# Optimization experiments

Measured on AMD Instinct MI355X. Metric: run time of the kernel, lower is better.

## Reference

```python
import jax, jax.numpy as jnp
import numpy as np

B, C, C2, E = 4, 1024, 1024, 1024
D = 1024          # context_size (d_q = d_kv)
NH = 16           # module's n_heads arg -> actual head_dim after the quirky view
G = D // NH       # effective number of head groups = 64


def setup_inputs() -> dict:
    key = jax.random.key(0)
    ks = jax.random.split(key, 6)
    s = 0.02
    return {
        "x1": jax.random.normal(ks[0], (B, C, E), dtype=jnp.float32),
        "x2": jax.random.normal(ks[1], (B, C2, E), dtype=jnp.float32),
        "W_q": jax.random.normal(ks[2], (E, D), dtype=jnp.float32) * s,
        "W_k": jax.random.normal(ks[3], (E, D), dtype=jnp.float32) * s,
        "W_v": jax.random.normal(ks[4], (E, D), dtype=jnp.float32) * s,
        "W_o": jax.random.normal(ks[5], (D, D), dtype=jnp.float32) * s,
    }


def _split_heads(t):
    # (B, S, D) -> view (B, S, G, NH) -> transpose(1,2) -> (B, G, S, NH)
    b, s, _ = t.shape
    return jnp.transpose(t.reshape(b, s, G, NH), (0, 2, 1, 3))


def reference(x1, x2, W_q, W_k, W_v, W_o):
    Q = _split_heads(x1 @ W_q)   # (B, G, C, NH)
    K = _split_heads(x2 @ W_k)   # (B, G, C2, NH)
    V = _split_heads(x2 @ W_v)   # (B, G, C2, NH)
    scale = 1.0 / jnp.sqrt(jnp.asarray(NH, dtype=Q.dtype))
    scores = jnp.einsum("bgqh,bgkh->bgqk", Q, K) * scale  # (B, G, C, C2)
    w = jax.nn.softmax(scores, axis=-1)
    out = jnp.einsum("bgqk,bgkh->bgqh", w, V)             # (B, G, C, NH)
    out = jnp.transpose(out, (0, 2, 1, 3)).reshape(B, C, D)
    return out @ W_o  # dropout p=0 -> identity
```

## Files before the change

### kernel.cpp

```cpp
#include <hip/hip_runtime.h>


typedef _Float16 f16x8 __attribute__((ext_vector_type(8)));
typedef _Float16 f16x4 __attribute__((ext_vector_type(4)));
typedef _Float16 f16x2 __attribute__((ext_vector_type(2)));
typedef float    f32x4 __attribute__((ext_vector_type(4)));
typedef float    f32x16 __attribute__((ext_vector_type(16)));

#define GLOAD_LDS16(gp, lp)                                              \
    __builtin_amdgcn_global_load_lds(                                    \
        (const __attribute__((address_space(1))) void*)(gp),             \
        (__attribute__((address_space(3))) void*)(lp), 16, 0, 0)

static __device__ __forceinline__ f16x8 pack8f(const float* p) {
    f16x2 a = __builtin_bit_cast(f16x2, __builtin_amdgcn_cvt_pkrtz(p[0], p[1]));
    f16x2 b = __builtin_bit_cast(f16x2, __builtin_amdgcn_cvt_pkrtz(p[2], p[3]));
    f16x2 c = __builtin_bit_cast(f16x2, __builtin_amdgcn_cvt_pkrtz(p[4], p[5]));
    f16x2 d = __builtin_bit_cast(f16x2, __builtin_amdgcn_cvt_pkrtz(p[6], p[7]));
    f16x8 r;
    r[0] = a[0]; r[1] = a[1]; r[2] = b[0]; r[3] = b[1];
    r[4] = c[0]; r[5] = c[1]; r[6] = d[0]; r[7] = d[1];
    return r;
}

__global__ __launch_bounds__(256) void prep_kernel(
        const float* __restrict__ x1, const float* __restrict__ x2,
        const float* __restrict__ W0, const float* __restrict__ W1,
        const float* __restrict__ W2, const float* __restrict__ W3,
        _Float16* __restrict__ y1, _Float16* __restrict__ y2,
        _Float16* __restrict__ T0, _Float16* __restrict__ T1,
        _Float16* __restrict__ T2, _Float16* __restrict__ T3) {
    int bx = blockIdx.x, tid = threadIdx.x;
    if (bx < 8192) {
        int i = bx * 256 + tid;
        const float* x = (i < 1048576) ? x1 : x2;
        _Float16* y = (i < 1048576) ? y1 : y2;
        int j = i & 1048575;
        float4 v = ((const float4*)x)[j];
        f16x4 h = { (_Float16)v.x, (_Float16)v.y, (_Float16)v.z, (_Float16)v.w };
        ((f16x4*)y)[j] = h;
    } else {
        int z = (bx - 8192) >> 10;
        const float* W = (z == 0) ? W0 : (z == 1) ? W1 : (z == 2) ? W2 : W3;
        _Float16* WT = (z == 0) ? T0 : (z == 1) ? T1 : (z == 2) ? T2 : T3;
        int t = (bx - 8192) & 1023;
        int c0 = (t & 31) * 32, r0 = (t >> 5) * 32;
        __shared__ float tile[32][33];
        int tx = tid & 31, ty = tid >> 5;
#pragma unroll
        for (int i = 0; i < 32; i += 8)
            tile[ty + i][tx] = W[(r0 + ty + i) * 1024 + (c0 + tx)];
        __syncthreads();
#pragma unroll
        for (int i = 0; i < 32; i += 8)
            WT[(c0 + ty + i) * 1024 + (r0 + tx)] = (_Float16)tile[tx][ty + i];
    }
}

template <int MT, bool OUTF32>
static __device__ __forceinline__ void gemm_body(const _Float16* __restrict__ Atile,
                                                 const _Float16* __restrict__ BTtile,
                                                 void* __restrict__ Ctile,
                                                 _Float16* As, _Float16* Bs) {
    constexpr int AF = MT / 32;
    const int tid = threadIdx.x, lane = tid & 63, wave = tid >> 6;
    const int wm = wave >> 1, wn = wave & 1;
    const int col = lane & 15, quad = lane >> 4;

    f32x4 acc[AF][4];
#pragma unroll
    for (int i = 0; i < AF; i++)
#pragma unroll
        for (int j = 0; j < 4; j++) acc[i][j] = (f32x4){0.f, 0.f, 0.f, 0.f};

    const int srow = wave * 8 + (lane >> 3);
    const int sch = (lane & 7) * 8;
    const _Float16* Ag = Atile + (size_t)srow * 1024 + sch;
    const _Float16* Bg = BTtile + (size_t)srow * 1024 + sch;
    _Float16* Asl = As + wave * 512;
    _Float16* Bsl = Bs + wave * 512;

    for (int kt = 0; kt < 16; kt++) {
        __syncthreads();
#pragma unroll
        for (int c = 0; c < AF; c++)
            GLOAD_LDS16(Ag + (size_t)(c * 32) * 1024 + kt * 64, Asl + c * 2048);
#pragma unroll
        for (int c = 0; c < 4; c++)
            GLOAD_LDS16(Bg + (size_t)(c * 32) * 1024 + kt * 64, Bsl + c * 2048);
        __syncthreads();
#pragma unroll
        for (int ki = 0; ki < 2; ki++) {
            f16x8 af[AF], bf[4];
#pragma unroll
            for (int i = 0; i < AF; i++)
                af[i] = *(const f16x8*)(As + (wm * (MT / 2) + i * 16 + col) * 64 + ki * 32 + quad * 8);
#pragma unroll
            for (int j = 0; j < 4; j++)
                bf[j] = *(const f16x8*)(Bs + (wn * 64 + j * 16 + col) * 64 + ki * 32 + quad * 8);
#pragma unroll
            for (int i = 0; i < AF; i++)
#pragma unroll
                for (int j = 0; j < 4; j++)
                    acc[i][j] = __builtin_amdgcn_mfma_f32_16x16x32_f16(af[i], bf[j], acc[i][j], 0, 0, 0);
        }
    }

#pragma unroll
    for (int i = 0; i < AF; i++)
#pragma unroll
        for (int ii = 0; ii < 4; ii++) {
            int row = wm * (MT / 2) + i * 16 + quad * 4 + ii;
#pragma unroll
            for (int j = 0; j < 4; j++) {
                int cc = wn * 64 + j * 16 + col;
                if (OUTF32) ((float*)Ctile)[(size_t)row * 1024 + cc] = acc[i][j][ii];
                else ((_Float16*)Ctile)[(size_t)row * 1024 + cc] = (_Float16)acc[i][j][ii];
            }
        }
}

__global__ __launch_bounds__(256, 3) void gemm_qkv_kernel(
        const _Float16* __restrict__ x1h, const _Float16* __restrict__ x2h,
        const _Float16* __restrict__ WqT, const _Float16* __restrict__ WkvT,
        _Float16* __restrict__ Qh, _Float16* __restrict__ Kh, _Float16* __restrict__ Vh) {
    __shared__ _Float16 As[128 * 64], Bs[128 * 64];
    int gx = blockIdx.x;
    const _Float16 *A, *BT;
    _Float16* C;
    int m0, n0;
    if (gx < 256) {
        m0 = (gx >> 3) * 128; n0 = (gx & 7) * 128;
        A = x1h; BT = WqT + (size_t)n0 * 1024; C = Qh + n0;
    } else {
        int idx = gx - 256;
        m0 = (idx >> 4) * 128;
        int nb = idx & 15;
        n0 = nb * 128;
        A = x2h; BT = WkvT + (size_t)n0 * 1024;
        C = (nb < 8) ? (Kh + n0) : (Vh + (n0 - 1024));
    }
    gemm_body<128, false>(A + (size_t)m0 * 1024, BT, (void*)(C + (size_t)m0 * 1024), As, Bs);
}

__global__ __launch_bounds__(256, 4) void gemm_wo_kernel(const _Float16* __restrict__ Ah,
                                                         const _Float16* __restrict__ WoT,
                                                         float* __restrict__ out) {
    __shared__ _Float16 As[64 * 64], Bs[128 * 64];
    int gx = blockIdx.x;
    int m0 = (gx >> 3) * 64, n0 = (gx & 7) * 128;
    gemm_body<64, true>(Ah + (size_t)m0 * 1024, WoT + (size_t)n0 * 1024,
                        (void*)(out + (size_t)m0 * 1024 + n0), As, Bs);
}

__global__ __launch_bounds__(256, 8) void attn_kernel(const _Float16* __restrict__ Qh,
                                                      const _Float16* __restrict__ Kh,
                                                      const _Float16* __restrict__ Vh,
                                                      _Float16* __restrict__ Ah) {
    int pair = blockIdx.y;
    int b = pair >> 6, g = pair & 63;
    __shared__ _Float16 KA[2048];
    __shared__ _Float16 VA[2048];
    __shared__ _Float16 ones[8];

    const _Float16* Kg = Kh + (size_t)(b * 1024) * 1024 + g * 16;
    const _Float16* Vg = Vh + (size_t)(b * 1024) * 1024 + g * 16;
    int tid = threadIdx.x;
    if (tid < 8) ones[tid] = (_Float16)1.f;

    int lane = tid & 63, wave = tid >> 6;
    int n = lane & 31, h5 = lane >> 5;
    int q0 = blockIdx.x * 128 + wave * 32;

    f16x8 qf;
    {
        f16x8 t = *(const f16x8*)(Qh + (size_t)(b * 1024 + q0 + n) * 1024 + g * 16 + h5 * 8);
#pragma unroll
        for (int j = 0; j < 8; j++) qf[j] = (_Float16)((float)t[j] * 0.360673760f);
    }

    f32x16 acc = {0.f, 0.f, 0.f, 0.f, 0.f, 0.f, 0.f, 0.f,
                  0.f, 0.f, 0.f, 0.f, 0.f, 0.f, 0.f, 0.f};
    const f32x16 zero16 = acc;

    const int krow = tid >> 1, kpart = tid & 1;
    const int kpm = (krow & 19) | ((krow & 4) << 1) | ((krow & 8) >> 1);
    const int kdst = (((krow >> 5) * 64) + kpm + 32 * kpart) * 8;
    const int vk0 = (tid >> 1) * 2 & 127, vpart = tid & 1;
    const int vbw2 = (((vk0 >> 4) * 256 + ((vk0 >> 3) & 1) * 128 + vpart * 64 + (vk0 & 7)))
                   ^ (((vk0 >> 3) & 7) << 3);

    int vaoff[8];
#pragma unroll
    for (int s = 0; s < 8; s++) {
        int nsw = (n & 8) | ((n & 7) ^ (((s & 3) << 1) | h5));
        vaoff[s] = (n < 16) ? ((s >> 2) * 1024 + (s & 3) * 256 + h5 * 128 + nsw * 8) : 0;
    }
    const _Float16* vrb = (n < 16) ? VA : ones;

    for (int c = 0; c < 8; c++) {
        if (c) __syncthreads();
        *(uint4*)(KA + kdst) =
            *(const uint4*)(Kg + (size_t)(c * 128 + krow) * 1024 + kpart * 8);
        if (tid < 128) {
            f16x8 v0 = *(const f16x8*)(Vg + (size_t)(c * 128 + vk0) * 1024 + vpart * 8);
            f16x8 v1 = *(const f16x8*)(Vg + (size_t)(c * 128 + vk0 + 1) * 1024 + vpart * 8);
#pragma unroll
            for (int j = 0; j < 8; j++) {
                f16x2 pr; pr[0] = v0[j]; pr[1] = v1[j];
                *(f16x2*)(VA + (vbw2 ^ (j * 8))) = pr;
            }
        }
        __syncthreads();

        __builtin_amdgcn_s_setprio(1);
#pragma unroll
        for (int t = 0; t < 4; t++) {
            f16x8 ak = *(const f16x8*)(KA + (t * 64 + lane) * 8);
            f32x16 s = __builtin_amdgcn_mfma_f32_32x32x16_f16(ak, qf, zero16, 0, 0, 0);
            float p[16];
#pragma unroll
            for (int i = 0; i < 16; i++) p[i] = __builtin_amdgcn_exp2f(s[i]);
            f16x8 pb0 = pack8f(p);
            f16x8 pb1 = pack8f(p + 8);
            f16x8 av0 = *(const f16x8*)(vrb + vaoff[2 * t]);
            f16x8 av1 = *(const f16x8*)(vrb + vaoff[2 * t + 1]);
            acc = __builtin_amdgcn_mfma_f32_32x32x16_f16(av0, pb0, acc, 0, 0, 0);
            acc = __builtin_amdgcn_mfma_f32_32x32x16_f16(av1, pb1, acc, 0, 0, 0);
        }
        __builtin_amdgcn_s_setprio(0);
    }

    float rl = 1.0f / acc[8];
    f16x4 o0, o1;
#pragma unroll
    for (int i = 0; i < 4; i++) o0[i] = (_Float16)(acc[i] * rl);
#pragma unroll
    for (int i = 0; i < 4; i++) o1[i] = (_Float16)(acc[4 + i] * rl);
    _Float16* ob = Ah + (size_t)(b * 1024 + q0 + n) * 1024 + g * 16 + h5 * 4;
    *(f16x4*)(ob) = o0;
    *(f16x4*)(ob + 8) = o1;
}

extern "C" void kernel_launch(void* const* d_in, const int* in_sizes, int n_in,
                              void* d_out, int out_size, void* d_ws, size_t ws_size,
                              hipStream_t stream) {
    const float* x1 = (const float*)d_in[0];
    const float* x2 = (const float*)d_in[1];
    const float* Wq = (const float*)d_in[2];
    const float* Wk = (const float*)d_in[3];
    const float* Wv = (const float*)d_in[4];
    const float* Wo = (const float*)d_in[5];

    char* ws = (char*)d_ws;
    const size_t MB = 1u << 20;
    if (ws_size < 56 * MB) return;

    _Float16* x1h = (_Float16*)(ws + 0 * MB);
    _Float16* x2h = (_Float16*)(ws + 8 * MB);
    _Float16* WqT = (_Float16*)(ws + 16 * MB);
    _Float16* WkT = (_Float16*)(ws + 18 * MB);
    _Float16* WvT = (_Float16*)(ws + 20 * MB);
    _Float16* WoT = (_Float16*)(ws + 22 * MB);
    _Float16* Qh  = (_Float16*)(ws + 24 * MB);
    _Float16* Kh  = (_Float16*)(ws + 32 * MB);
    _Float16* Vh  = (_Float16*)(ws + 40 * MB);
    _Float16* Ah  = (_Float16*)(ws + 48 * MB);

    prep_kernel<<<12288, 256, 0, stream>>>(x1, x2, Wq, Wk, Wv, Wo,
                                           x1h, x2h, WqT, WkT, WvT, WoT);

    gemm_qkv_kernel<<<768, 256, 0, stream>>>(x1h, x2h, WqT, WkT, Qh, Kh, Vh);

    attn_kernel<<<dim3(8, 256), 256, 0, stream>>>(Qh, Kh, Vh, Ah);

    gemm_wo_kernel<<<512, 256, 0, stream>>>(Ah, WoT, (float*)d_out);
}
```

Before: 197.1 us.

## Double-buffer K/V tiles in attention with 512-thread blocks and async K loads

The attention kernel now uses 512-thread blocks, so each block covers 256 queries and reuses the staged K/V chunk across twice as many query rows. K and V chunks are double-buffered in LDS. K is fetched with direct global-to-LDS loads by the first half of the threads, while the second half prefetches V into registers during compute and transposes it into the alternate buffer afterwards, leaving one barrier per chunk. This is meant to hide global load latency and halve the K/V traffic per query, at the cost of doubled LDS use, a lower occupancy bound, and per-iteration swizzled offset arithmetic.

New measurement: 192.1 us. -2.5%, faster.

```diff
diff --git a/kernel.cpp b/kernel.cpp
--- a/kernel.cpp
+++ b/kernel.cpp
@@ -153,14 +153,14 @@
                         (void*)(out + (size_t)m0 * 1024 + n0), As, Bs);
 }
 
-__global__ __launch_bounds__(256, 8) void attn_kernel(const _Float16* __restrict__ Qh,
+__global__ __launch_bounds__(512, 6) void attn_kernel(const _Float16* __restrict__ Qh,
                                                       const _Float16* __restrict__ Kh,
                                                       const _Float16* __restrict__ Vh,
                                                       _Float16* __restrict__ Ah) {
     int pair = blockIdx.y;
     int b = pair >> 6, g = pair & 63;
-    __shared__ _Float16 KA[2048];
-    __shared__ _Float16 VA[2048];
+    __shared__ _Float16 KA[4096];
+    __shared__ _Float16 VA[4096];
     __shared__ _Float16 ones[8];
 
     const _Float16* Kg = Kh + (size_t)(b * 1024) * 1024 + g * 16;
@@ -170,7 +170,7 @@
 
     int lane = tid & 63, wave = tid >> 6;
     int n = lane & 31, h5 = lane >> 5;
-    int q0 = blockIdx.x * 128 + wave * 32;
+    int q0 = blockIdx.x * 256 + wave * 32;
 
     f16x8 qf;
     {
@@ -183,52 +183,79 @@
                   0.f, 0.f, 0.f, 0.f, 0.f, 0.f, 0.f, 0.f};
     const f32x16 zero16 = acc;
 
-    const int krow = tid >> 1, kpart = tid & 1;
-    const int kpm = (krow & 19) | ((krow & 4) << 1) | ((krow & 8) >> 1);
-    const int kdst = (((krow >> 5) * 64) + kpm + 32 * kpart) * 8;
-    const int vk0 = (tid >> 1) * 2 & 127, vpart = tid & 1;
-    const int vbw2 = (((vk0 >> 4) * 256 + ((vk0 >> 3) & 1) * 128 + vpart * 64 + (vk0 & 7)))
-                   ^ (((vk0 >> 3) & 7) << 3);
-
-    int vaoff[8];
-#pragma unroll
-    for (int s = 0; s < 8; s++) {
-        int nsw = (n & 8) | ((n & 7) ^ (((s & 3) << 1) | h5));
-        vaoff[s] = (n < 16) ? ((s >> 2) * 1024 + (s & 3) * 256 + h5 * 128 + nsw * 8) : 0;
-    }
+    const int pl = lane & 31;
+    const int kperm = (pl & 19) | ((pl & 4) << 1) | ((pl & 8) >> 1);
+    const _Float16* ksrc = Kg + (size_t)((wave & 3) * 32 + kperm) * 1024 + (lane >> 5) * 8;
+    _Float16* kdst = KA + (wave & 3) * 512;
+
+    const int u = tid & 255;
+    const int vk0 = (u & 63) * 2;
+    const int hq = u >> 6;
+    const int vpart = hq >> 1, jb = (hq & 1) * 4;
+    const _Float16* vsrcA = Vg + (size_t)vk0 * 1024 + vpart * 8 + jb;
+    const int vbw3 = ((((vk0 >> 4) * 256) + ((vk0 >> 3) & 1) * 128 + vpart * 64 + (vk0 & 7))
+                      ^ (((vk0 >> 3) & 7) << 3)) ^ (jb * 8);
+
+    const int vb0 = h5 * 128 + ((n & 8) | ((n & 7) ^ h5)) * 8;
+    const int vmask = (n < 16) ? -1 : 0;
     const _Float16* vrb = (n < 16) ? VA : ones;
+    const int vbufstep = (n < 16) ? 2048 : 0;
+
+    if (tid < 256) {
+        GLOAD_LDS16(ksrc, kdst);
+    } else {
+        f16x4 va = *(const f16x4*)(vsrcA);
+        f16x4 vb = *(const f16x4*)(vsrcA + 1024);
+#pragma unroll
+        for (int jj = 0; jj < 4; jj++) {
+            f16x2 pr; pr[0] = va[jj]; pr[1] = vb[jj];
+            *(f16x2*)(VA + (vbw3 ^ (jj * 8))) = pr;
+        }
+    }
 
     for (int c = 0; c < 8; c++) {
-        if (c) __syncthreads();
-        *(uint4*)(KA + kdst) =
-            *(const uint4*)(Kg + (size_t)(c * 128 + krow) * 1024 + kpart * 8);
-        if (tid < 128) {
-            f16x8 v0 = *(const f16x8*)(Vg + (size_t)(c * 128 + vk0) * 1024 + vpart * 8);
-            f16x8 v1 = *(const f16x8*)(Vg + (size_t)(c * 128 + vk0 + 1) * 1024 + vpart * 8);
-#pragma unroll
-            for (int j = 0; j < 8; j++) {
-                f16x2 pr; pr[0] = v0[j]; pr[1] = v1[j];
-                *(f16x2*)(VA + (vbw2 ^ (j * 8))) = pr;
+        __syncthreads();
+        const int cb = c & 1;
+        f16x4 va, vb;
+        if (c < 7) {
+            if (tid < 256) {
+                GLOAD_LDS16(ksrc + (size_t)((c + 1) * 128) * 1024, kdst + (cb ^ 1) * 2048);
+            } else {
+                va = *(const f16x4*)(vsrcA + (size_t)((c + 1) * 128) * 1024);
+                vb = *(const f16x4*)(vsrcA + (size_t)((c + 1) * 128) * 1024 + 1024);
             }
         }
-        __syncthreads();
+        const _Float16* akc = KA + cb * 2048;
+        const _Float16* vrbc = vrb + cb * vbufstep;
 
         __builtin_amdgcn_s_setprio(1);
 #pragma unroll
         for (int t = 0; t < 4; t++) {
-            f16x8 ak = *(const f16x8*)(KA + (t * 64 + lane) * 8);
+            f16x8 ak = *(const f16x8*)(akc + (t * 64 + lane) * 8);
             f32x16 s = __builtin_amdgcn_mfma_f32_32x32x16_f16(ak, qf, zero16, 0, 0, 0);
             float p[16];
 #pragma unroll
             for (int i = 0; i < 16; i++) p[i] = __builtin_amdgcn_exp2f(s[i]);
             f16x8 pb0 = pack8f(p);
             f16x8 pb1 = pack8f(p + 8);
-            f16x8 av0 = *(const f16x8*)(vrb + vaoff[2 * t]);
-            f16x8 av1 = *(const f16x8*)(vrb + vaoff[2 * t + 1]);
+            const int o0 = ((vb0 ^ (((2 * t) & 3) << 4)) | (((2 * t) & 3) << 8)
+                            | (((2 * t) >> 2) << 10)) & vmask;
+            const int o1 = ((vb0 ^ (((2 * t + 1) & 3) << 4)) | (((2 * t + 1) & 3) << 8)
+                            | (((2 * t + 1) >> 2) << 10)) & vmask;
+            f16x8 av0 = *(const f16x8*)(vrbc + o0);
+            f16x8 av1 = *(const f16x8*)(vrbc + o1);
             acc = __builtin_amdgcn_mfma_f32_32x32x16_f16(av0, pb0, acc, 0, 0, 0);
             acc = __builtin_amdgcn_mfma_f32_32x32x16_f16(av1, pb1, acc, 0, 0, 0);
         }
         __builtin_amdgcn_s_setprio(0);
+
+        if (c < 7 && tid >= 256) {
+#pragma unroll
+            for (int jj = 0; jj < 4; jj++) {
+                f16x2 pr; pr[0] = va[jj]; pr[1] = vb[jj];
+                *(f16x2*)(VA + (cb ^ 1) * 2048 + (vbw3 ^ (jj * 8))) = pr;
+            }
+        }
     }
 
     float rl = 1.0f / acc[8];
@@ -272,7 +299,7 @@
 
     gemm_qkv_kernel<<<768, 256, 0, stream>>>(x1h, x2h, WqT, WkT, Qh, Kh, Vh);
 
-    attn_kernel<<<dim3(8, 256), 256, 0, stream>>>(Qh, Kh, Vh, Ah);
+    attn_kernel<<<dim3(4, 256), 512, 0, stream>>>(Qh, Kh, Vh, Ah);
 
     gemm_wo_kernel<<<512, 256, 0, stream>>>(Ah, WoT, (float*)d_out);
 }
```
